# Optimization experiments

Measured on AMD Instinct MI355X. Metric: run time of the kernel, lower is better.

The kernel has to match this reference:

```python
import jax, jax.numpy as jnp
import numpy as np

N, E, G, H = 50000, 800000, 2048, 128
DIS = 3  # dis_emb is None -> raw frac_diff (3 dims)
EIN = 2 * H + 6 + DIS  # 265


def _lin_init(key, fan_in, fan_out):
    lim = 1.0 / np.sqrt(fan_in)
    return jax.random.uniform(key, (fan_in, fan_out), jnp.float32, -lim, lim)


def setup_inputs() -> dict:
    key = jax.random.key(0)
    ks = jax.random.split(key, 12)
    node_features = jax.random.normal(ks[0], (N, H), jnp.float32)
    frac_coords = jax.random.uniform(ks[1], (N, 3), jnp.float32)
    lattices = jax.random.normal(ks[2], (G, 6), jnp.float32)
    frac_diff = jax.random.normal(ks[3], (E, 3), jnp.float32)
    edge_index = jax.random.randint(ks[4], (2, E), 0, N, jnp.int64 if jax.config.jax_enable_x64 else jnp.int32)
    edge2graph = jax.random.randint(ks[5], (E,), 0, G, edge_index.dtype)
    return dict(
        node_features=node_features,
        frac_coords=frac_coords,
        lattices=lattices,
        frac_diff=frac_diff,
        edge_index=edge_index,
        edge2graph=edge2graph,
        e_w1=_lin_init(ks[6], EIN, H), e_b1=jnp.zeros((H,), jnp.float32),
        e_w2=_lin_init(ks[7], H, H), e_b2=jnp.zeros((H,), jnp.float32),
        n_w1=_lin_init(ks[8], 2 * H, H), n_b1=jnp.zeros((H,), jnp.float32),
        n_w2=_lin_init(ks[9], H, H), n_b2=jnp.zeros((H,), jnp.float32),
    )


def reference(node_features, frac_coords, lattices, frac_diff, edge_index, edge2graph,
              e_w1, e_b1, e_w2, e_b2, n_w1, n_b1, n_w2, n_b2):
    n_nodes = node_features.shape[0]
    silu = jax.nn.silu
    # edge model: gather endpoints, concat with per-graph lattice + frac_diff
    hi = node_features[edge_index[0]]            # [E, H]
    hj = node_features[edge_index[1]]            # [E, H]
    lat = lattices[edge2graph]                   # [E, 6]
    edges_input = jnp.concatenate([hi, hj, lat, frac_diff], axis=1)  # [E, 265]
    e = silu(edges_input @ e_w1 + e_b1)
    edge_features = silu(e @ e_w2 + e_b2)        # [E, H]
    # scatter-mean aggregate onto source nodes
    seg = edge_index[0]
    agg_sum = jax.ops.segment_sum(edge_features, seg, num_segments=n_nodes)
    cnt = jax.ops.segment_sum(jnp.ones((edge_features.shape[0],), edge_features.dtype), seg, num_segments=n_nodes)
    agg = agg_sum / jnp.maximum(cnt, 1.0)[:, None]
    # node model + residual
    h = jnp.concatenate([node_features, agg], axis=1)  # [N, 2H]
    h = silu(h @ n_w1 + n_b1)
    node_output = silu(h @ n_w2 + n_b2)
    return node_features + node_output
```

## Files before the change

kernel.cpp:

```cpp
#include <hip/hip_runtime.h>

#define N_NODES 50000
#define N_EDGES 800000
#define HDIM 128
#define N_GRAPH 2048

typedef __bf16 bf16x8 __attribute__((ext_vector_type(8)));
typedef float f32x4 __attribute__((ext_vector_type(4)));
typedef float f32x16 __attribute__((ext_vector_type(16)));

static __device__ __forceinline__ unsigned short f2bf(float f) {
    unsigned int u = __float_as_uint(f);
    u += 0x7fffu + ((u >> 16) & 1u);
    return (unsigned short)(u >> 16);
}
static __device__ __forceinline__ float bflo(unsigned int u) { return __uint_as_float(u << 16); }
static __device__ __forceinline__ float bfhi(unsigned int u) { return __uint_as_float(u & 0xFFFF0000u); }

static __device__ __forceinline__ unsigned int cvt_pk_bf16(float lo, float hi) {
    unsigned int r;
    asm("v_cvt_pk_bf16_f32 %0, %1, %2" : "=v"(r) : "v"(lo), "v"(hi));
    return r;
}

static __device__ __forceinline__ float silu_f(float x) {
    float e = __builtin_amdgcn_exp2f(x * -1.44269504f);
    return x * __builtin_amdgcn_rcpf(1.0f + e);
}

#define PREP_BLOCKS 1408
#define HIST_BLOCKS 3125
#define ZERO_BLOCKS 6250
__global__ void prep_hist_kernel(const float* __restrict__ ew1, const float* __restrict__ ew2,
                                 const float* __restrict__ nw1, const float* __restrict__ nw2,
                                 const float* __restrict__ eb1, const float* __restrict__ lattices,
                                 const int* __restrict__ eidx,
                                 unsigned short* __restrict__ W1aT, unsigned short* __restrict__ W1bT,
                                 unsigned short* __restrict__ W2t, unsigned short* __restrict__ N1t,
                                 unsigned short* __restrict__ N2t, unsigned short* __restrict__ Lb,
                                 int* __restrict__ buf, float* __restrict__ agg) {
    const int bid = blockIdx.x;
    if (bid >= PREP_BLOCKS + HIST_BLOCKS) {
        const int idx = (bid - PREP_BLOCKS - HIST_BLOCKS) * 256 + threadIdx.x;
        ((float4*)agg)[idx] = make_float4(0.f, 0.f, 0.f, 0.f);
        return;
    }
    if (bid >= PREP_BLOCKS) {
        int e = (bid - PREP_BLOCKS) * 256 + threadIdx.x;
        if (e < N_EDGES) atomicAdd(&buf[eidx[e]], 1);
        return;
    }
    int i = bid * 256 + threadIdx.x;
    if (i < 16384) {
        int n = i >> 7, k = i & 127;
        W1aT[i] = f2bf(ew1[k * 128 + n]);
    } else if (i < 32768) {
        int j = i - 16384; int n = j >> 7, k = j & 127;
        W1bT[j] = f2bf(ew1[(128 + k) * 128 + n]);
    } else if (i < 49152) {
        int j = i - 32768; int n = j >> 7, k = j & 127;
        W2t[j] = f2bf(ew2[k * 128 + n]);
    } else if (i < 81920) {
        int j = i - 49152; int n = j >> 8, k = j & 255;
        N1t[j] = f2bf(nw1[k * 128 + n]);
    } else if (i < 98304) {
        int j = i - 81920; int n = j >> 7, k = j & 127;
        N2t[j] = f2bf(nw2[k * 128 + n]);
    } else if (i < 98304 + 262144) {
        int j = i - 98304; int g = j >> 7, c = j & 127;
        float s = eb1[c];
#pragma unroll
        for (int t = 0; t < 6; ++t) s += lattices[g * 6 + t] * ew1[(256 + t) * 128 + c];
        Lb[j] = f2bf(s);
    }
}

__global__ __launch_bounds__(1024) void scan_kernel(int* __restrict__ buf) {
    constexpr int CH = 12288;
    __shared__ int lds[CH];
    __shared__ int wpart[16];
    __shared__ int carry_s;
    const int t = threadIdx.x;
    const int wave = t >> 6, lane = t & 63;
    if (t == 0) carry_s = 0;
    __syncthreads();
#pragma unroll 1
    for (int base = 0; base < N_NODES; base += CH) {
#pragma unroll
        for (int k = 0; k < CH / 1024; ++k) {
            int f = k * 1024 + t;
            lds[f] = (base + f < N_NODES) ? buf[base + f] : 0;
        }
        __syncthreads();
        int loc[12];
        int s = 0;
#pragma unroll
        for (int i = 0; i < 12; ++i) { loc[i] = lds[t * 12 + i]; s += loc[i]; }
        int ps = s;
#pragma unroll
        for (int off = 1; off < 64; off <<= 1) {
            int v = __shfl_up(ps, off);
            if (lane >= off) ps += v;
        }
        if (lane == 63) wpart[wave] = ps;
        __syncthreads();
        if (t == 0) {
            int r = carry_s;
#pragma unroll
            for (int i = 0; i < 16; ++i) { int v = wpart[i]; wpart[i] = r; r += v; }
            carry_s = r;
        }
        __syncthreads();
        int run = wpart[wave] + (ps - s);
#pragma unroll
        for (int i = 0; i < 12; ++i) { int tmp = loc[i]; lds[t * 12 + i] = run; run += tmp; }
        __syncthreads();
#pragma unroll
        for (int k = 0; k < CH / 1024; ++k) {
            int f = k * 1024 + t;
            if (base + f < N_NODES) buf[base + f] = lds[f];
        }
        __syncthreads();
    }
}

#define PERM_BLOCKS2 3125
#define PQ_BLOCKS ((N_NODES + 63) / 64)
__global__ __launch_bounds__(256, 4) void perm_pq_kernel(
    const int* __restrict__ eidx, const int* __restrict__ e2g,
    const float* __restrict__ frac_diff, int* __restrict__ buf,
    unsigned short* __restrict__ perm_lo, unsigned char* __restrict__ perm_hi,
    uint4* __restrict__ rec, const int packed,
    const float* __restrict__ nf, const unsigned short* __restrict__ W1aT,
    const unsigned short* __restrict__ W1bT,
    unsigned short* __restrict__ P, unsigned short* __restrict__ Qm) {
    constexpr int SA = 136;
    __shared__ unsigned short sm[64 * SA];
    const int bid = blockIdx.x;
    const int tid = threadIdx.x;

    if (bid < PERM_BLOCKS2) {
        int e = bid * 256 + tid;
        if (e < N_EDGES) {
            int s = eidx[e];
            int pos = atomicAdd(&buf[s], 1);
            if (packed) {
                int d = eidx[N_EDGES + e];
                int g = e2g[e];
                unsigned int w0 = (unsigned int)s | ((unsigned int)d << 16);
                unsigned int w1 = (unsigned int)g | ((unsigned int)f2bf(frac_diff[3 * e]) << 16);
                unsigned int w2 = (unsigned int)f2bf(frac_diff[3 * e + 1]) |
                                  ((unsigned int)f2bf(frac_diff[3 * e + 2]) << 16);
                rec[pos] = make_uint4(w0, w1, w2, 0u);
            } else {
                perm_lo[pos] = (unsigned short)(e & 0xFFFF);
                perm_hi[pos] = (unsigned char)(e >> 16);
            }
        }
        return;
    }

    const int n0 = (bid - PERM_BLOCKS2) * 64;
    const int mrow = tid >> 2, q = tid & 3;
    {
        const int node = n0 + mrow;
        unsigned short* row = sm + mrow * SA + q * 32;
        if (node < N_NODES) {
            const float4* a4 = (const float4*)(nf + (size_t)node * HDIM) + q * 8;
#pragma unroll
            for (int j = 0; j < 8; ++j) {
                float4 v = a4[j];
                *(ushort4*)(row + 4 * j) = make_ushort4(f2bf(v.x), f2bf(v.y), f2bf(v.z), f2bf(v.w));
            }
        } else {
#pragma unroll
            for (int j = 0; j < 8; ++j) *(ushort4*)(row + 4 * j) = make_ushort4(0, 0, 0, 0);
        }
    }
    __syncthreads();

    const int wave = tid >> 6, lane = tid & 63;
    const int lr = lane & 15, kq = lane >> 4;
    f32x4 acca[8] = {}, accb[8] = {};
    const int arow = (wave * 16 + lr) * SA;
#pragma unroll
    for (int ks = 0; ks < 128; ks += 32) {
        bf16x8 a = *(const bf16x8*)(sm + arow + ks + kq * 8);
#pragma unroll
        for (int nt = 0; nt < 8; ++nt) {
            bf16x8 ba = *(const bf16x8*)(W1aT + (nt * 16 + lr) * 128 + ks + kq * 8);
            acca[nt] = __builtin_amdgcn_mfma_f32_16x16x32_bf16(a, ba, acca[nt], 0, 0, 0);
            bf16x8 bb = *(const bf16x8*)(W1bT + (nt * 16 + lr) * 128 + ks + kq * 8);
            accb[nt] = __builtin_amdgcn_mfma_f32_16x16x32_bf16(a, bb, accb[nt], 0, 0, 0);
        }
    }
    __syncthreads();

    const int node = n0 + mrow;
#pragma unroll
    for (int nt = 0; nt < 8; ++nt) {
        const int col = nt * 16 + lr;
#pragma unroll
        for (int r = 0; r < 4; ++r)
            sm[(wave * 16 + kq * 4 + r) * SA + col] = f2bf(acca[nt][r]);
    }
    __syncthreads();
    if (node < N_NODES) {
        uint4* dst = (uint4*)(P + (size_t)node * HDIM + q * 32);
        const uint4* srcp = (const uint4*)(sm + mrow * SA + q * 32);
#pragma unroll
        for (int j = 0; j < 4; ++j) dst[j] = srcp[j];
    }
    __syncthreads();
#pragma unroll
    for (int nt = 0; nt < 8; ++nt) {
        const int col = nt * 16 + lr;
#pragma unroll
        for (int r = 0; r < 4; ++r)
            sm[(wave * 16 + kq * 4 + r) * SA + col] = f2bf(accb[nt][r]);
    }
    __syncthreads();
    if (node < N_NODES) {
        uint4* dst = (uint4*)(Qm + (size_t)node * HDIM + q * 32);
        const uint4* srcp = (const uint4*)(sm + mrow * SA + q * 32);
#pragma unroll
        for (int j = 0; j < 4; ++j) dst[j] = srcp[j];
    }
}


static __device__ __forceinline__ void build_afrag(
    const uint4* pu, const uint4* qu, const uint4* lu,
    float f0, float f1, float f2,
    const unsigned int* wlds, int hi, bf16x8* afrag) {
#pragma unroll
    for (int kk = 0; kk < 8; ++kk) {
        const unsigned int* wl = wlds + (kk * 2 + hi) * 12;
        const uint4 w0v = *(const uint4*)(wl);
        const uint4 w1v = *(const uint4*)(wl + 4);
        const uint4 w2v = *(const uint4*)(wl + 8);
        const unsigned int* pw = (const unsigned int*)&pu[kk];
        const unsigned int* qw = (const unsigned int*)&qu[kk];
        const unsigned int* lw = (const unsigned int*)&lu[kk];
        const unsigned int* w0w = (const unsigned int*)&w0v;
        const unsigned int* w1w = (const unsigned int*)&w1v;
        const unsigned int* w2w = (const unsigned int*)&w2v;
        unsigned int ow[4];
#pragma unroll
        for (int w = 0; w < 4; ++w) {
            float x0 = bflo(pw[w]) + bflo(qw[w]) + bflo(lw[w])
                     + f0 * bflo(w0w[w]) + f1 * bflo(w1w[w]) + f2 * bflo(w2w[w]);
            float x1 = bfhi(pw[w]) + bfhi(qw[w]) + bfhi(lw[w])
                     + f0 * bfhi(w0w[w]) + f1 * bfhi(w1w[w]) + f2 * bfhi(w2w[w]);
            ow[w] = cvt_pk_bf16(silu_f(x0), silu_f(x1));
        }
        afrag[kk] = *(bf16x8*)ow;
    }
}

static __device__ __forceinline__ void do_mfma(
    const bf16x8* afrag, const unsigned short* __restrict__ W2t,
    int row, int hi, f32x16* acc) {
#pragma unroll
    for (int kk = 0; kk < 8; ++kk) {
#pragma unroll
        for (int t4 = 0; t4 < 4; ++t4) {
            bf16x8 bb = *(const bf16x8*)(W2t + (t4 * 32 + row) * 128 + kk * 16 + hi * 8);
            acc[t4] = __builtin_amdgcn_mfma_f32_32x32x16_bf16(afrag[kk], bb, acc[t4], 0, 0, 0);
        }
    }
}

static __device__ __forceinline__ void epilogue(
    const f32x16* acc, const int* sc, const int* snq,
    int row, int hi, const float* __restrict__ b2, float* __restrict__ agg) {
#pragma unroll
    for (int t4 = 0; t4 < 4; ++t4) {
        const int col = t4 * 32 + row;
        const float bias = b2[col];
        float p[16], tq[4], to[4];
#pragma unroll
        for (int rq = 0; rq < 4; ++rq) {
            float s0 = silu_f(acc[t4][4 * rq + 0] + bias);
            float s1 = silu_f(acc[t4][4 * rq + 1] + bias);
            float s2 = silu_f(acc[t4][4 * rq + 2] + bias);
            float s3 = silu_f(acc[t4][4 * rq + 3] + bias);
            p[4 * rq + 0] = s0;
            p[4 * rq + 1] = s0 + s1;
            p[4 * rq + 2] = p[4 * rq + 1] + s2;
            p[4 * rq + 3] = p[4 * rq + 2] + s3;
            tq[rq] = p[4 * rq + 3];
            to[rq] = __shfl_xor(tq[rq], 32);
        }
        float cum = 0.f;
#pragma unroll
        for (int rq = 0; rq < 4; ++rq) {
            const float off = cum + (hi ? to[rq] : 0.f);
            cum += tq[rq] + to[rq];
#pragma unroll
            for (int i = 0; i < 4; ++i) {
                const int r = 4 * rq + i;
                const float val = p[r] + off;
                const int myrow = 4 * (2 * rq + hi) + i;
                const bool lastg = (myrow == 31);
                const int nxt = (i < 3) ? sc[r + 1] : snq[rq];
                const bool bnd = lastg || (sc[r] != nxt);
                if (bnd) {
                    atomicAdd(&agg[(size_t)sc[r] * HDIM + col], val);
                    if (!lastg) atomicAdd(&agg[(size_t)nxt * HDIM + col], -val);
                }
            }
        }
    }
}

#define EDGE_NWG (N_EDGES / 256)
template <bool PACKED>
static __device__ __forceinline__ void fetch_meta(
    int i, const uint4* __restrict__ rec, const int* __restrict__ eidx,
    const int* __restrict__ e2g, const float* __restrict__ frac_diff,
    const unsigned short* __restrict__ perm_lo, const unsigned char* __restrict__ perm_hi,
    int& src, int& dst, int& g, float& f0, float& f1, float& f2) {
    if (PACKED) {
        const uint4 rv = rec[i];
        src = rv.x & 0xFFFF;
        dst = rv.x >> 16;
        g = rv.y & 0xFFFF;
        f0 = bfhi(rv.y);
        f1 = bflo(rv.z);
        f2 = bfhi(rv.z);
    } else {
        const int e = (int)perm_lo[i] | ((int)perm_hi[i] << 16);
        src = eidx[e];
        dst = eidx[N_EDGES + e];
        g = e2g[e];
        f0 = frac_diff[3 * e];
        f1 = frac_diff[3 * e + 1];
        f2 = frac_diff[3 * e + 2];
    }
}

static __device__ __forceinline__ void gather_pq(
    const unsigned short* __restrict__ P, const unsigned short* __restrict__ Qm,
    int src, int dst, int hi, uint4* pu, uint4* qu) {
    const size_t pr = (size_t)src * HDIM, qr = (size_t)dst * HDIM;
#pragma unroll
    for (int kk = 0; kk < 8; ++kk) {
        const int c0 = kk * 16 + hi * 8;
        pu[kk] = *(const uint4*)(P + pr + c0);
        qu[kk] = *(const uint4*)(Qm + qr + c0);
    }
}

static __device__ __forceinline__ void gather_l(
    const unsigned short* __restrict__ Lb, int g, int hi, uint4* lu) {
    const size_t lr = (size_t)g * HDIM;
#pragma unroll
    for (int kk = 0; kk < 8; ++kk) {
        const int c0 = kk * 16 + hi * 8;
        lu[kk] = *(const uint4*)(Lb + lr + c0);
    }
}

static __device__ __forceinline__ void make_sc(int src, int hi, int* sc, int* snq) {
#pragma unroll
    for (int r = 0; r < 16; ++r) sc[r] = __shfl(src, (r & 3) + 8 * (r >> 2) + 4 * hi);
#pragma unroll
    for (int j = 0; j < 4; ++j) snq[j] = __shfl(src, (4 * (2 * j + hi) + 4) & 31);
}

template <bool PACKED>
__global__ __launch_bounds__(256, 2) void edge_kernel(
    const unsigned short* __restrict__ P, const unsigned short* __restrict__ Qm,
    const unsigned short* __restrict__ Lb, const float* __restrict__ frac_diff,
    const int* __restrict__ eidx, const int* __restrict__ e2g,
    const unsigned short* __restrict__ perm_lo, const unsigned char* __restrict__ perm_hi,
    const uint4* __restrict__ rec,
    const float* __restrict__ e_w1, const unsigned short* __restrict__ W2t,
    const float* __restrict__ b2, float* __restrict__ agg) {
    __shared__ __align__(16) unsigned int wlds[192];
    const int tid = threadIdx.x;
    {
        const float* wrbase = e_w1 + 262 * HDIM;
        if (tid < 192) {
            const int w = tid & 3, rw = (tid >> 2) % 3, hi = (tid / 12) & 1, kk = tid / 24;
            const int c = kk * 16 + hi * 8 + 2 * w;
            wlds[((kk * 2 + hi) * 3 + rw) * 4 + w] =
                (unsigned int)f2bf(wrbase[rw * HDIM + c]) |
                ((unsigned int)f2bf(wrbase[rw * HDIM + c + 1]) << 16);
        }
    }
    __syncthreads();

    const int wv = tid >> 6, lane = tid & 63;
    const int row = lane & 31, hi = lane >> 5;
    const int base = (blockIdx.x * 4 + wv) * 64;

    int srcA, dstA, gA; float fA0, fA1, fA2;
    fetch_meta<PACKED>(base + row, rec, eidx, e2g, frac_diff, perm_lo, perm_hi,
                       srcA, dstA, gA, fA0, fA1, fA2);
    int srcB, dstB, gB; float fB0, fB1, fB2;
    fetch_meta<PACKED>(base + 32 + row, rec, eidx, e2g, frac_diff, perm_lo, perm_hi,
                       srcB, dstB, gB, fB0, fB1, fB2);

    uint4 puA[8], quA[8], luA[8];
    gather_pq(P, Qm, srcA, dstA, hi, puA, quA);
    gather_l(Lb, gA, hi, luA);
    uint4 puB[8], quB[8];
    gather_pq(P, Qm, srcB, dstB, hi, puB, quB);

    uint4 luB[8];
    {
        bf16x8 afrag[8];
        build_afrag(puA, quA, luA, fA0, fA1, fA2, wlds, hi, afrag);
        int sc[16], snq[4];
        make_sc(srcA, hi, sc, snq);
        f32x16 acc[4] = {};
        do_mfma(afrag, W2t, row, hi, acc);
        int gB_pin = gB;
        asm volatile("" : "+v"(gB_pin));
        gather_l(Lb, gB_pin, hi, luB);
        epilogue(acc, sc, snq, row, hi, b2, agg);
    }

    {
        bf16x8 afrag[8];
        build_afrag(puB, quB, luB, fB0, fB1, fB2, wlds, hi, afrag);
        int sc[16], snq[4];
        make_sc(srcB, hi, sc, snq);
        f32x16 acc[4] = {};
        do_mfma(afrag, W2t, row, hi, acc);
        epilogue(acc, sc, snq, row, hi, b2, agg);
    }
}

__global__ __launch_bounds__(256, 4) void node_kernel(
    const float* __restrict__ nf, const float* __restrict__ agg,
    const int* __restrict__ buf,
    const unsigned short* __restrict__ N1t, const float* __restrict__ b1,
    const unsigned short* __restrict__ N2t, const float* __restrict__ b2,
    float* __restrict__ out) {
    constexpr int SA = 264;
    constexpr int S2 = 136;
    constexpr int SFo = 132;
    __shared__ unsigned short sm[64 * SA];
    float* smf = (float*)sm;

    const int tid = threadIdx.x;
    const int n0 = blockIdx.x * 64;
    const int mrow = tid >> 2, q = tid & 3;
    {
        const int node = n0 + mrow;
        unsigned short* row = sm + mrow * SA;
        const int cbq = q * 32;
        if (node < N_NODES) {
            const int c = buf[node] - (node ? buf[node - 1] : 0);
            const float inv = 1.0f / (float)max(c, 1);
            const float4* a4 = (const float4*)(nf + (size_t)node * HDIM) + q * 8;
            const float4* g4 = (const float4*)(agg + (size_t)node * HDIM) + q * 8;
#pragma unroll
            for (int j = 0; j < 8; ++j) {
                float4 v = a4[j];
                *(ushort4*)(row + cbq + 4 * j) =
                    make_ushort4(f2bf(v.x), f2bf(v.y), f2bf(v.z), f2bf(v.w));
                float4 g = g4[j];
                *(ushort4*)(row + HDIM + cbq + 4 * j) =
                    make_ushort4(f2bf(g.x * inv), f2bf(g.y * inv), f2bf(g.z * inv), f2bf(g.w * inv));
            }
        } else {
#pragma unroll
            for (int j = 0; j < 8; ++j) {
                *(ushort4*)(row + cbq + 4 * j) = make_ushort4(0, 0, 0, 0);
                *(ushort4*)(row + HDIM + cbq + 4 * j) = make_ushort4(0, 0, 0, 0);
            }
        }
    }
    __syncthreads();

    const int wave = tid >> 6, lane = tid & 63;
    const int lr = lane & 15, kq = lane >> 4;

    f32x4 acc[8] = {};
    const int arow = (wave * 16 + lr) * SA;
#pragma unroll
    for (int ks = 0; ks < 256; ks += 32) {
        bf16x8 a = *(const bf16x8*)(sm + arow + ks + kq * 8);
#pragma unroll
        for (int nt = 0; nt < 8; ++nt) {
            bf16x8 bb = *(const bf16x8*)(N1t + (nt * 16 + lr) * 256 + ks + kq * 8);
            acc[nt] = __builtin_amdgcn_mfma_f32_16x16x32_bf16(a, bb, acc[nt], 0, 0, 0);
        }
    }
    __syncthreads();

#pragma unroll
    for (int nt = 0; nt < 8; ++nt) {
        const int col = nt * 16 + lr;
        const float bias = b1[col];
#pragma unroll
        for (int r = 0; r < 4; ++r) {
            const int mm = wave * 16 + kq * 4 + r;
            sm[mm * S2 + col] = f2bf(silu_f(acc[nt][r] + bias));
        }
    }
    __syncthreads();

    f32x4 acc2[8] = {};
    const int arow2 = (wave * 16 + lr) * S2;
#pragma unroll
    for (int ks = 0; ks < 128; ks += 32) {
        bf16x8 a = *(const bf16x8*)(sm + arow2 + ks + kq * 8);
#pragma unroll
        for (int nt = 0; nt < 8; ++nt) {
            bf16x8 bb = *(const bf16x8*)(N2t + (nt * 16 + lr) * 128 + ks + kq * 8);
            acc2[nt] = __builtin_amdgcn_mfma_f32_16x16x32_bf16(a, bb, acc2[nt], 0, 0, 0);
        }
    }
    __syncthreads();

#pragma unroll
    for (int nt = 0; nt < 8; ++nt) {
        const int col = nt * 16 + lr;
        const float bias = b2[col];
#pragma unroll
        for (int r = 0; r < 4; ++r) {
            const int mm = wave * 16 + kq * 4 + r;
            smf[mm * SFo + col] = silu_f(acc2[nt][r] + bias);
        }
    }
    __syncthreads();
    {
        const int node = n0 + mrow;
        if (node < N_NODES) {
            const float4* nfr = (const float4*)(nf + (size_t)node * HDIM) + q * 8;
            float4* outr = (float4*)(out + (size_t)node * HDIM) + q * 8;
            const float* st = smf + mrow * SFo + q * 32;
#pragma unroll
            for (int j = 0; j < 8; ++j) {
                float4 v = nfr[j];
                float4 s4 = *(const float4*)(st + 4 * j);
                v.x += s4.x; v.y += s4.y; v.z += s4.z; v.w += s4.w;
                outr[j] = v;
            }
        }
    }
}

extern "C" void kernel_launch(void* const* d_in, const int* in_sizes, int n_in,
                              void* d_out, int out_size, void* d_ws, size_t ws_size,
                              hipStream_t stream) {
    const float* node_features = (const float*)d_in[0];
    const float* lattices = (const float*)d_in[2];
    const float* frac_diff = (const float*)d_in[3];
    const int* edge_index = (const int*)d_in[4];
    const int* edge2graph = (const int*)d_in[5];
    const float* e_w1 = (const float*)d_in[6];
    const float* e_b1 = (const float*)d_in[7];
    const float* e_w2 = (const float*)d_in[8];
    const float* e_b2 = (const float*)d_in[9];
    const float* n_w1 = (const float*)d_in[10];
    const float* n_b1 = (const float*)d_in[11];
    const float* n_w2 = (const float*)d_in[12];
    const float* n_b2 = (const float*)d_in[13];

    char* ws = (char*)d_ws;
    unsigned short* W1aT = (unsigned short*)(ws);
    unsigned short* W1bT = (unsigned short*)(ws + 32768);
    unsigned short* W2t  = (unsigned short*)(ws + 65536);
    unsigned short* N1t  = (unsigned short*)(ws + 98304);
    unsigned short* N2t  = (unsigned short*)(ws + 163840);
    unsigned short* Lb   = (unsigned short*)(ws + 196608);
    unsigned short* P    = (unsigned short*)(ws + 720896);
    unsigned short* Qm   = (unsigned short*)(ws + 13520896);
    int* buf             = (int*)(ws + 26320896);
    unsigned short* perm_lo = (unsigned short*)(ws + 26520896);
    unsigned char* perm_hi  = (unsigned char*)(ws + 28120896);
    uint4* rec           = (uint4*)(ws + 28920896);
    float* agg = (float*)d_out;

    const int packed = (ws_size >= 28920896 + (size_t)N_EDGES * 16) ? 1 : 0;

    hipMemsetAsync(buf, 0, (size_t)N_NODES * 4, stream);

    prep_hist_kernel<<<PREP_BLOCKS + HIST_BLOCKS + ZERO_BLOCKS, 256, 0, stream>>>(
        e_w1, e_w2, n_w1, n_w2, e_b1, lattices, edge_index,
        W1aT, W1bT, W2t, N1t, N2t, Lb, buf, agg);

    scan_kernel<<<1, 1024, 0, stream>>>(buf);

    perm_pq_kernel<<<PERM_BLOCKS2 + PQ_BLOCKS, 256, 0, stream>>>(
        edge_index, edge2graph, frac_diff, buf, perm_lo, perm_hi, rec, packed,
        node_features, W1aT, W1bT, P, Qm);

    if (packed) {
        edge_kernel<true><<<EDGE_NWG, 256, 0, stream>>>(
            P, Qm, Lb, frac_diff, edge_index, edge2graph, perm_lo, perm_hi, rec,
            e_w1, W2t, e_b2, agg);
    } else {
        edge_kernel<false><<<EDGE_NWG, 256, 0, stream>>>(
            P, Qm, Lb, frac_diff, edge_index, edge2graph, perm_lo, perm_hi, rec,
            e_w1, W2t, e_b2, agg);
    }

    node_kernel<<<(N_NODES + 63) / 64, 256, 0, stream>>>(
        node_features, agg, buf, N1t, n_b1, N2t, n_b2, (float*)d_out);
}
```

Measured before the change: 502.3 us.

## Parallelize prefix scan across blocks and defer second edge-tile gather

Replaces the single-block serial prefix scan over node counts with a two-kernel multi-block scan: per-block scans write block totals, then a second pass adds the prefix offsets. The goal is to remove the latency of one workgroup walking 50k entries in chunks. Separately, in the edge kernel the gather of P/Q rows for the second 32-edge tile now happens after the first tile's MFMA instead of up front. This lowers peak register pressure but starts those loads later. The extra kernel launch adds some overhead.

```diff
diff --git a/kernel.cpp b/kernel.cpp
--- a/kernel.cpp
+++ b/kernel.cpp
@@ -75,53 +75,46 @@
     }
 }
 
-__global__ __launch_bounds__(1024) void scan_kernel(int* __restrict__ buf) {
-    constexpr int CH = 12288;
-    __shared__ int lds[CH];
+#define SCAN_BLOCKS ((N_NODES + 1023) / 1024)
+__device__ int scan_aux_g[64];
+
+__global__ __launch_bounds__(1024) void scan1_kernel(int* __restrict__ buf) {
     __shared__ int wpart[16];
-    __shared__ int carry_s;
     const int t = threadIdx.x;
+    const int i = blockIdx.x * 1024 + t;
     const int wave = t >> 6, lane = t & 63;
-    if (t == 0) carry_s = 0;
-    __syncthreads();
-#pragma unroll 1
-    for (int base = 0; base < N_NODES; base += CH) {
-#pragma unroll
-        for (int k = 0; k < CH / 1024; ++k) {
-            int f = k * 1024 + t;
-            lds[f] = (base + f < N_NODES) ? buf[base + f] : 0;
-        }
-        __syncthreads();
-        int loc[12];
-        int s = 0;
-#pragma unroll
-        for (int i = 0; i < 12; ++i) { loc[i] = lds[t * 12 + i]; s += loc[i]; }
-        int ps = s;
-#pragma unroll
-        for (int off = 1; off < 64; off <<= 1) {
-            int v = __shfl_up(ps, off);
-            if (lane >= off) ps += v;
-        }
-        if (lane == 63) wpart[wave] = ps;
-        __syncthreads();
-        if (t == 0) {
-            int r = carry_s;
-#pragma unroll
-            for (int i = 0; i < 16; ++i) { int v = wpart[i]; wpart[i] = r; r += v; }
-            carry_s = r;
-        }
-        __syncthreads();
-        int run = wpart[wave] + (ps - s);
-#pragma unroll
-        for (int i = 0; i < 12; ++i) { int tmp = loc[i]; lds[t * 12 + i] = run; run += tmp; }
-        __syncthreads();
-#pragma unroll
-        for (int k = 0; k < CH / 1024; ++k) {
-            int f = k * 1024 + t;
-            if (base + f < N_NODES) buf[base + f] = lds[f];
-        }
-        __syncthreads();
-    }
+    int v = (i < N_NODES) ? buf[i] : 0;
+    int ps = v;
+#pragma unroll
+    for (int off = 1; off < 64; off <<= 1) {
+        int u = __shfl_up(ps, off);
+        if (lane >= off) ps += u;
+    }
+    if (lane == 63) wpart[wave] = ps;
+    __syncthreads();
+    if (t == 0) {
+        int r = 0;
+#pragma unroll
+        for (int k = 0; k < 16; ++k) { int u = wpart[k]; wpart[k] = r; r += u; }
+        scan_aux_g[blockIdx.x] = r;
+    }
+    __syncthreads();
+    if (i < N_NODES) buf[i] = wpart[wave] + (ps - v);
+}
+
+__global__ __launch_bounds__(1024) void scan2_kernel(int* __restrict__ buf) {
+    const int t = threadIdx.x;
+    const int b = blockIdx.x;
+    __shared__ int off_s;
+    if (t < 64) {
+        int v = (t < b) ? scan_aux_g[t] : 0;
+#pragma unroll
+        for (int o = 32; o > 0; o >>= 1) v += __shfl_down(v, o);
+        if (t == 0) off_s = v;
+    }
+    __syncthreads();
+    const int i = b * 1024 + t;
+    if (b > 0 && i < N_NODES) buf[i] += off_s;
 }
 
 #define PERM_BLOCKS2 3125
@@ -406,10 +399,8 @@
     uint4 puA[8], quA[8], luA[8];
     gather_pq(P, Qm, srcA, dstA, hi, puA, quA);
     gather_l(Lb, gA, hi, luA);
-    uint4 puB[8], quB[8];
-    gather_pq(P, Qm, srcB, dstB, hi, puB, quB);
-
-    uint4 luB[8];
+
+    uint4 puB[8], quB[8], luB[8];
     {
         bf16x8 afrag[8];
         build_afrag(puA, quA, luA, fA0, fA1, fA2, wlds, hi, afrag);
@@ -417,8 +408,9 @@
         make_sc(srcA, hi, sc, snq);
         f32x16 acc[4] = {};
         do_mfma(afrag, W2t, row, hi, acc);
-        int gB_pin = gB;
-        asm volatile("" : "+v"(gB_pin));
+        int sB = srcB, dB = dstB, gB_pin = gB;
+        asm volatile("" : "+v"(sB), "+v"(dB), "+v"(gB_pin));
+        gather_pq(P, Qm, sB, dB, hi, puB, quB);
         gather_l(Lb, gB_pin, hi, luB);
         epilogue(acc, sc, snq, row, hi, b2, agg);
     }
@@ -586,7 +578,8 @@
         e_w1, e_w2, n_w1, n_w2, e_b1, lattices, edge_index,
         W1aT, W1bT, W2t, N1t, N2t, Lb, buf, agg);
 
-    scan_kernel<<<1, 1024, 0, stream>>>(buf);
+    scan1_kernel<<<SCAN_BLOCKS, 1024, 0, stream>>>(buf);
+    scan2_kernel<<<SCAN_BLOCKS, 1024, 0, stream>>>(buf);
 
     perm_pq_kernel<<<PERM_BLOCKS2 + PQ_BLOCKS, 256, 0, stream>>>(
         edge_index, edge2graph, frac_diff, buf, perm_lo, perm_hi, rec, packed,
```

Result: faster. 484.7 us, median of 3 (-3.5%).
